# Optimization experiments

Hardware: AMD Instinct MI355X
Metric: run time of the kernel (lower is better)

The kernel has to match this reference:

```python
import jax, jax.numpy as jnp
import numpy as np

N_NODES = 100000
N_EDGES = 1600000
NUM_GRAPHS = 64
HID = 32
EPS = 1e-5


def _seg_max0(x, ids, num_segments):
    # segment max; segments with no entries become 0 (PyG-style identity)
    m = jax.ops.segment_max(x, ids, num_segments=num_segments)
    return jnp.where(jnp.isfinite(m), m, 0.0)


def _pointnet_layer(h, pos, src, dst, W1, b1, W2, b2):
    # message: mlp(cat([h_j, pos_j - pos_i])) ; aggregate: max at target i
    edge_feat = jnp.concatenate([h[src], pos[src] - pos[dst]], axis=-1)  # [E, C+3]
    m = jnp.maximum(edge_feat @ W1 + b1, 0.0) @ W2 + b2                  # [E, out]
    return _seg_max0(m, dst, N_NODES)                                    # [N, out]


def _batchnorm(x, gamma, beta):
    # training-mode BatchNorm1d: batch stats, biased variance
    mu = jnp.mean(x, axis=0)
    var = jnp.mean((x - mu) ** 2, axis=0)
    return (x - mu) * jax.lax.rsqrt(var + EPS) * gamma + beta


def setup_inputs() -> dict:
    key = jax.random.key(0)
    ks = jax.random.split(key, 16)
    pos = jax.random.normal(ks[0], (N_NODES, 3), dtype=jnp.float32)
    edge_index = jax.random.randint(ks[1], (2, N_EDGES), 0, N_NODES, dtype=jnp.int64)
    batch = jnp.sort(jax.random.randint(ks[2], (N_NODES,), 0, NUM_GRAPHS, dtype=jnp.int64))

    def lin(k, fan_in, fan_out):
        lim = 1.0 / np.sqrt(fan_in)
        kw, kb = jax.random.split(k)
        W = jax.random.uniform(kw, (fan_in, fan_out), jnp.float32, -lim, lim)
        b = jax.random.uniform(kb, (fan_out,), jnp.float32, -lim, lim)
        return W, b

    W1a, b1a = lin(ks[3], 3 + 3, HID)
    W2a, b2a = lin(ks[4], HID, HID)
    W1b, b1b = lin(ks[5], HID + 3, 2 * HID)
    W2b, b2b = lin(ks[6], 2 * HID, 2 * HID)
    Wc, bc = lin(ks[7], 2 * HID, 2)
    return {
        'pos': pos, 'edge_index': edge_index, 'batch': batch,
        'W1a': W1a, 'b1a': b1a, 'W2a': W2a, 'b2a': b2a,
        'g1': jnp.ones((HID,), jnp.float32), 'beta1': jnp.zeros((HID,), jnp.float32),
        'W1b': W1b, 'b1b': b1b, 'W2b': W2b, 'b2b': b2b,
        'g2': jnp.ones((2 * HID,), jnp.float32), 'beta2': jnp.zeros((2 * HID,), jnp.float32),
        'Wc': Wc, 'bc': bc,
    }


def reference(pos, edge_index, batch, W1a, b1a, W2a, b2a, g1, beta1,
              W1b, b1b, W2b, b2b, g2, beta2, Wc, bc):
    src, dst = edge_index[0], edge_index[1]  # source j -> target i
    h = _pointnet_layer(pos, pos, src, dst, W1a, b1a, W2a, b2a)   # [N, 32]
    h = jnp.maximum(_batchnorm(h, g1, beta1), 0.0)
    h = _pointnet_layer(h, pos, src, dst, W1b, b1b, W2b, b2b)     # [N, 64]
    h = jnp.maximum(_batchnorm(h, g2, beta2), 0.0)
    g = _seg_max0(h, batch, NUM_GRAPHS)                            # [G, 64]
    return g @ Wc + bc                                             # [G, 2]
```

## Files before the change

### kernel.cpp

```cpp
#include <hip/hip_runtime.h>

#define NN 100000
#define NE 1600000
#define NG 64
#define BSZ 98
#define NBUK 1021
#define SENTROW 127
#define NBLK1 391
#define EPB 4096

typedef __attribute__((ext_vector_type(8))) short bf16x8;
typedef __attribute__((ext_vector_type(4))) float f32x4;

union AFrag { bf16x8 v; uint4 u; };

__device__ __forceinline__ bool finitef(float v) {
    return (__float_as_uint(v) & 0x7F800000u) != 0x7F800000u;
}
__device__ __forceinline__ unsigned short f2bf(float f) {
    unsigned int u = __float_as_uint(f);
    u += 0x7fffu + ((u >> 16) & 1u);
    return (unsigned short)(u >> 16);
}
__device__ __forceinline__ unsigned int cvtpk(float lo, float hi) {
    unsigned int r;
    asm("v_cvt_pk_bf16_f32 %0, %1, %2" : "=v"(r) : "v"(lo), "v"(hi));
    return r;
}
__device__ __forceinline__ float bflo(unsigned int q) { return __uint_as_float(q << 16); }
__device__ __forceinline__ float bfhi(unsigned int q) { return __uint_as_float(q & 0xffff0000u); }

__device__ __forceinline__ unsigned int enc(float f) {
    unsigned int u = __float_as_uint(f);
    return (u & 0x80000000u) ? ~u : (u | 0x80000000u);
}
__device__ __forceinline__ float dec(unsigned int k) {
    unsigned int u = (k & 0x80000000u) ? (k ^ 0x80000000u) : ~k;
    return __uint_as_float(u);
}

__global__ __launch_bounds__(256) void p1count(const int* __restrict__ dst,
                                               int* __restrict__ gmat) {
    __shared__ int h[NBUK];
    int tid = threadIdx.x;
    for (int i = tid; i < NBUK; i += 256) h[i] = 0;
    __syncthreads();
    int e0 = blockIdx.x * EPB;
    #pragma unroll
    for (int i = 0; i < 16; ++i) {
        int e = e0 + tid + i * 256;
        if (e < NE) atomicAdd(&h[dst[e] / BSZ], 1);
    }
    __syncthreads();
    for (int i = tid; i < NBUK; i += 256) gmat[blockIdx.x * NBUK + i] = h[i];
}

__global__ __launch_bounds__(512) void scanA(int* __restrict__ gmat, int* __restrict__ tot) {
    __shared__ int ls[512];
    int b = blockIdx.x, tid = threadIdx.x;
    int v = (tid < NBLK1) ? gmat[tid * NBUK + b] : 0;
    ls[tid] = v;
    __syncthreads();
    for (int o = 1; o < 512; o <<= 1) {
        int t = (tid >= o) ? ls[tid - o] : 0;
        __syncthreads();
        ls[tid] += t;
        __syncthreads();
    }
    if (tid < NBLK1) gmat[tid * NBUK + b] = ls[tid] - v;
    if (tid == 511) tot[b] = ls[511];
}

__global__ __launch_bounds__(1024) void scanB(const int* __restrict__ tot,
        int* __restrict__ base,
        unsigned int* __restrict__ gmax, unsigned int* __restrict__ gneg) {
    __shared__ int ls[1024];
    int tid = threadIdx.x;
    int v = (tid < NBUK) ? tot[tid] : 0;
    ls[tid] = v;
    __syncthreads();
    for (int o = 1; o < 1024; o <<= 1) {
        int t = (tid >= o) ? ls[tid - o] : 0;
        __syncthreads();
        ls[tid] += t;
        __syncthreads();
    }
    if (tid < NBUK) base[tid] = ls[tid] - v;
    if (tid == 1023) base[NBUK] = ls[1023];
    for (int i = tid; i < NG * 64; i += 1024) { gmax[i] = 0u; gneg[i] = 0u; }
}

__global__ __launch_bounds__(256) void p1scatter(const int* __restrict__ src,
        const int* __restrict__ dst, const int* __restrict__ gmat,
        const int* __restrict__ base, int* __restrict__ sedge) {
    __shared__ int cur[NBUK];
    int tid = threadIdx.x;
    for (int i = tid; i < NBUK; i += 256) cur[i] = base[i] + gmat[blockIdx.x * NBUK + i];
    __syncthreads();
    int e0 = blockIdx.x * EPB;
    #pragma unroll
    for (int i = 0; i < 16; ++i) {
        int e = e0 + tid + i * 256;
        if (e < NE) {
            int d = dst[e];
            int buk = d / BSZ;
            int row = d - buk * BSZ;
            int p = atomicAdd(&cur[buk], 1);
            sedge[p] = src[e] | (row << 20);
        }
    }
}

__global__ __launch_bounds__(256) void uA_kernel(const float* __restrict__ pos,
        const float* __restrict__ W1, const float* __restrict__ b1,
        unsigned short* __restrict__ PA, unsigned short* __restrict__ QA) {
    __shared__ float sWp[96], sWq[96], sb[32];
    if (threadIdx.x < 96) {
        float wt = W1[96 + threadIdx.x];
        sWq[threadIdx.x] = wt;
        sWp[threadIdx.x] = W1[threadIdx.x] + wt;
    }
    if (threadIdx.x < 32) sb[threadIdx.x] = b1[threadIdx.x];
    __syncthreads();
    int n = blockIdx.x * 256 + threadIdx.x;
    if (n >= NN) return;
    float p0 = pos[n * 3 + 0], p1 = pos[n * 3 + 1], p2 = pos[n * 3 + 2];
    float P[32], Q[32];
    #pragma unroll
    for (int c = 0; c < 32; ++c) {
        P[c] = fmaf(p2, sWp[64 + c], fmaf(p1, sWp[32 + c], fmaf(p0, sWp[c], sb[c])));
        Q[c] = fmaf(p2, sWq[64 + c], fmaf(p1, sWq[32 + c], p0 * sWq[c]));
    }
    uint4* po = (uint4*)(PA + (size_t)n * 32);
    uint4* qo = (uint4*)(QA + (size_t)n * 32);
    #pragma unroll
    for (int q = 0; q < 4; ++q) {
        po[q] = make_uint4(cvtpk(P[8*q],P[8*q+1]), cvtpk(P[8*q+2],P[8*q+3]),
                           cvtpk(P[8*q+4],P[8*q+5]), cvtpk(P[8*q+6],P[8*q+7]));
        qo[q] = make_uint4(cvtpk(Q[8*q],Q[8*q+1]), cvtpk(Q[8*q+2],Q[8*q+3]),
                           cvtpk(Q[8*q+4],Q[8*q+5]), cvtpk(Q[8*q+6],Q[8*q+7]));
    }
}

__global__ __launch_bounds__(256) void uB_kernel(const unsigned int* __restrict__ accA,
        const float* __restrict__ ssA, const float* __restrict__ pos,
        const float* __restrict__ W1, const float* __restrict__ b1,
        unsigned short* __restrict__ PB, unsigned short* __restrict__ QB) {
    __shared__ float sW[32 * 64];
    __shared__ float sWt[3 * 64];
    __shared__ float sb[64];
    for (int i = threadIdx.x; i < 32 * 64; i += 256) sW[i] = W1[i];
    if (threadIdx.x < 192) sWt[threadIdx.x] = W1[32 * 64 + threadIdx.x];
    if (threadIdx.x < 64) sb[threadIdx.x] = b1[threadIdx.x];
    __syncthreads();
    int n = blockIdx.x * 256 + threadIdx.x;
    if (n >= NN) return;
    float h[32];
    const uint4* a4 = (const uint4*)(accA + (size_t)n * 32);
    #pragma unroll
    for (int q = 0; q < 8; ++q) {
        uint4 v = a4[q];
        unsigned int vv[4] = {v.x, v.y, v.z, v.w};
        #pragma unroll
        for (int r = 0; r < 4; ++r) {
            int c = 4 * q + r;
            float x = dec(vv[r]);
            x = finitef(x) ? x : 0.f;
            h[c] = fmaxf(fmaf(x, ssA[c], ssA[32 + c]), 0.f);
        }
    }
    float p0 = pos[n * 3 + 0], p1 = pos[n * 3 + 1], p2 = pos[n * 3 + 2];
    float Q[64], P[64];
    #pragma unroll
    for (int c = 0; c < 64; ++c) {
        Q[c] = fmaf(p2, sWt[128 + c], fmaf(p1, sWt[64 + c], p0 * sWt[c]));
        P[c] = Q[c] + sb[c];
    }
    #pragma unroll
    for (int k = 0; k < 32; ++k) {
        float x = h[k];
        #pragma unroll
        for (int c = 0; c < 64; ++c) P[c] = fmaf(x, sW[k * 64 + c], P[c]);
    }
    uint4* po = (uint4*)(PB + (size_t)n * 64);
    uint4* qo = (uint4*)(QB + (size_t)n * 64);
    #pragma unroll
    for (int q = 0; q < 8; ++q) {
        po[q] = make_uint4(cvtpk(P[8*q],P[8*q+1]), cvtpk(P[8*q+2],P[8*q+3]),
                           cvtpk(P[8*q+4],P[8*q+5]), cvtpk(P[8*q+6],P[8*q+7]));
        qo[q] = make_uint4(cvtpk(Q[8*q],Q[8*q+1]), cvtpk(Q[8*q+2],Q[8*q+3]),
                           cvtpk(Q[8*q+4],Q[8*q+5]), cvtpk(Q[8*q+6],Q[8*q+7]));
    }
}

__global__ __launch_bounds__(256, 6) void edgeA(
        const unsigned short* __restrict__ PA, const unsigned short* __restrict__ QA,
        const int* __restrict__ sedge, const int* __restrict__ bbase,
        const float* __restrict__ W2, const float* __restrict__ b2,
        unsigned int* __restrict__ accA, float* __restrict__ partials) {
    __shared__ __align__(16) short w2f[2 * 64 * 8];
    __shared__ unsigned int nm[32 * 99];
    __shared__ float psum[256], psq[256];

    const int tid = threadIdx.x;
    const int b   = blockIdx.x;
    const int nb0 = b * BSZ;
    const int lane = tid & 63, wv = tid >> 6;
    const int kg = lane >> 4;

    #pragma unroll
    for (int ii = 0; ii < 4; ++ii) {
        int i = tid + ii * 256;
        int j = i & 7, ln = (i >> 3) & 63, t = (i >> 9) & 1;
        int k = ((ln >> 4) & 3) * 8 + j, col = (ln & 15) + 16 * t;
        w2f[i] = (short)f2bf(W2[k * 32 + col]);
    }
    for (int i = tid; i < 32 * 99; i += 256) nm[i] = 0;
    __syncthreads();

    float b2v[2];
    #pragma unroll
    for (int t = 0; t < 2; ++t) b2v[t] = b2[(lane & 15) + 16 * t];

    const int bs = bbase[b], be = bbase[b + 1];
    int idx = bs + wv * 64 + lane;
    int myed = (idx < be) ? sedge[idx] : (SENTROW << 20);
    for (int e0 = bs; e0 < be; e0 += 256) {
        int nxt = (idx + 256 < be) ? sedge[idx + 256] : (SENTROW << 20);
        idx += 256;

        int edg[4]; unsigned int rw4[4];
        #pragma unroll
        for (int g = 0; g < 4; ++g) {
            edg[g] = __shfl(myed, g * 16 + (lane & 15), 64);
            unsigned int p = 0;
            #pragma unroll
            for (int r = 0; r < 4; ++r) {
                int e2 = __shfl(myed, g * 16 + kg * 4 + r, 64);
                p |= ((unsigned int)(e2 >> 20) & 0xFFu) << (8 * r);
            }
            rw4[g] = p;
        }

        AFrag af[4];
        #pragma unroll
        for (int g = 0; g < 4; ++g) {
            int s = edg[g] & 0xFFFFF;
            int rq = min(edg[g] >> 20, BSZ - 1);
            uint4 Pq = *(const uint4*)&PA[(size_t)s * 32 + kg * 8];
            uint4 Qq = *(const uint4*)&QA[(size_t)(nb0 + rq) * 32 + kg * 8];
            unsigned int pu[4] = {Pq.x, Pq.y, Pq.z, Pq.w};
            unsigned int qu[4] = {Qq.x, Qq.y, Qq.z, Qq.w};
            unsigned int outw[4];
            #pragma unroll
            for (int p = 0; p < 4; ++p) {
                float vlo = fmaxf(bflo(pu[p]) - bflo(qu[p]), 0.f);
                float vhi = fmaxf(bfhi(pu[p]) - bfhi(qu[p]), 0.f);
                outw[p] = cvtpk(vlo, vhi);
            }
            af[g].u = make_uint4(outw[0], outw[1], outw[2], outw[3]);
        }

        #pragma unroll
        for (int t = 0; t < 2; ++t) {
            bf16x8 bfr = *(const bf16x8*)&w2f[(t * 64 + lane) * 8];
            int ch = t * 16 + (lane & 15);
            #pragma unroll
            for (int g = 0; g < 4; ++g) {
                f32x4 c = {b2v[t], b2v[t], b2v[t], b2v[t]};
                f32x4 acc = __builtin_amdgcn_mfma_f32_16x16x32_bf16(af[g].v, bfr, c, 0, 0, 0);
                #pragma unroll
                for (int r = 0; r < 4; ++r) {
                    int rr = (rw4[g] >> (8 * r)) & 0xFF;
                    if (rr < BSZ) atomicMax(&nm[ch * 99 + rr], enc(acc[r]));
                }
            }
        }
        myed = nxt;
    }

    __syncthreads();
    {
        int c = tid & 31, sub = tid >> 5;
        float s = 0.f, q = 0.f;
        for (int nl = sub; nl < BSZ; nl += 8) {
            int n = nb0 + nl;
            if (n >= NN) break;
            unsigned int k = nm[c * 99 + nl];
            accA[(size_t)n * 32 + c] = k;
            float v = dec(k);
            v = finitef(v) ? v : 0.f;
            s += v; q = fmaf(v, v, q);
        }
        psum[tid] = s; psq[tid] = q;
    }
    __syncthreads();
    if (tid < 128) { psum[tid] += psum[tid + 128]; psq[tid] += psq[tid + 128]; }
    __syncthreads();
    if (tid < 64)  { psum[tid] += psum[tid + 64];  psq[tid] += psq[tid + 64]; }
    __syncthreads();
    if (tid < 32) {
        partials[b * 64 + tid]      = psum[tid] + psum[tid + 32];
        partials[b * 64 + 32 + tid] = psq[tid]  + psq[tid + 32];
    }
}

__global__ __launch_bounds__(256, 4) void edgeB(
        const unsigned short* __restrict__ PB, const unsigned short* __restrict__ QB,
        const int* __restrict__ sedge, const int* __restrict__ bbase,
        const int* __restrict__ batch,
        const float* __restrict__ W2, const float* __restrict__ b2,
        float* __restrict__ partials,
        unsigned int* __restrict__ gmax, unsigned int* __restrict__ gneg) {
    __shared__ __align__(16) short w2f[2 * 4 * 64 * 8];
    __shared__ unsigned int nm[64 * 99];
    __shared__ float psum[256], psq[256];

    const int tid = threadIdx.x;
    const int b   = blockIdx.x;
    const int nb0 = b * BSZ;
    const int lane = tid & 63, wv = tid >> 6;
    const int kg = lane >> 4;

    #pragma unroll
    for (int ii = 0; ii < 16; ++ii) {
        int i = tid + ii * 256;
        int j = i & 7, ln = (i >> 3) & 63, t = (i >> 9) & 3, ks = (i >> 11) & 1;
        int k = ks * 32 + ((ln >> 4) & 3) * 8 + j, col = (ln & 15) + 16 * t;
        w2f[i] = (short)f2bf(W2[k * 64 + col]);
    }
    for (int i = tid; i < 64 * 99; i += 256) nm[i] = 0;
    __syncthreads();

    float b2v[4];
    #pragma unroll
    for (int t = 0; t < 4; ++t) b2v[t] = b2[(lane & 15) + 16 * t];

    const int bs = bbase[b], be = bbase[b + 1];
    int idx = bs + wv * 64 + lane;
    int myed = (idx < be) ? sedge[idx] : (SENTROW << 20);
    for (int e0 = bs; e0 < be; e0 += 256) {
        int nxt = (idx + 256 < be) ? sedge[idx + 256] : (SENTROW << 20);
        idx += 256;

        int edg[4]; unsigned int rw4[4];
        #pragma unroll
        for (int g = 0; g < 4; ++g) {
            edg[g] = __shfl(myed, g * 16 + (lane & 15), 64);
            unsigned int p = 0;
            #pragma unroll
            for (int r = 0; r < 4; ++r) {
                int e2 = __shfl(myed, g * 16 + kg * 4 + r, 64);
                p |= ((unsigned int)(e2 >> 20) & 0xFFu) << (8 * r);
            }
            rw4[g] = p;
        }

        AFrag af[4][2];
        #pragma unroll
        for (int g = 0; g < 4; ++g) {
            int s = edg[g] & 0xFFFFF;
            int rq = min(edg[g] >> 20, BSZ - 1);
            #pragma unroll
            for (int ks = 0; ks < 2; ++ks) {
                uint4 Pq = *(const uint4*)&PB[(size_t)s * 64 + ks * 32 + kg * 8];
                uint4 Qq = *(const uint4*)&QB[(size_t)(nb0 + rq) * 64 + ks * 32 + kg * 8];
                unsigned int pu[4] = {Pq.x, Pq.y, Pq.z, Pq.w};
                unsigned int qu[4] = {Qq.x, Qq.y, Qq.z, Qq.w};
                unsigned int outw[4];
                #pragma unroll
                for (int p = 0; p < 4; ++p) {
                    float vlo = fmaxf(bflo(pu[p]) - bflo(qu[p]), 0.f);
                    float vhi = fmaxf(bfhi(pu[p]) - bfhi(qu[p]), 0.f);
                    outw[p] = cvtpk(vlo, vhi);
                }
                af[g][ks].u = make_uint4(outw[0], outw[1], outw[2], outw[3]);
            }
        }

        #pragma unroll
        for (int t = 0; t < 4; ++t) {
            bf16x8 bf0 = *(const bf16x8*)&w2f[((0 * 4 + t) * 64 + lane) * 8];
            bf16x8 bf1 = *(const bf16x8*)&w2f[((1 * 4 + t) * 64 + lane) * 8];
            int ch = t * 16 + (lane & 15);
            #pragma unroll
            for (int g = 0; g < 4; ++g) {
                f32x4 c = {b2v[t], b2v[t], b2v[t], b2v[t]};
                c = __builtin_amdgcn_mfma_f32_16x16x32_bf16(af[g][0].v, bf0, c, 0, 0, 0);
                f32x4 acc = __builtin_amdgcn_mfma_f32_16x16x32_bf16(af[g][1].v, bf1, c, 0, 0, 0);
                #pragma unroll
                for (int r = 0; r < 4; ++r) {
                    int rr = (rw4[g] >> (8 * r)) & 0xFF;
                    if (rr < BSZ) atomicMax(&nm[ch * 99 + rr], enc(acc[r]));
                }
            }
        }
        myed = nxt;
    }

    __syncthreads();
    {
        int c = tid & 63, sub = tid >> 6;
        float s = 0.f, q = 0.f;
        float rmax = 0.f, rneg = 0.f; int curg = -1;
        for (int nl = sub; nl < BSZ; nl += 4) {
            int n = nb0 + nl;
            if (n >= NN) break;
            float v = dec(nm[c * 99 + nl]);
            v = finitef(v) ? v : 0.f;
            s += v; q = fmaf(v, v, q);
            int g = batch[n];
            if (g != curg) {
                if (curg >= 0) {
                    atomicMax(&gmax[curg * 64 + c], enc(rmax));
                    atomicMax(&gneg[curg * 64 + c], enc(rneg));
                }
                curg = g; rmax = v; rneg = -v;
            } else {
                rmax = fmaxf(rmax, v); rneg = fmaxf(rneg, -v);
            }
        }
        if (curg >= 0) {
            atomicMax(&gmax[curg * 64 + c], enc(rmax));
            atomicMax(&gneg[curg * 64 + c], enc(rneg));
        }
        psum[tid] = s; psq[tid] = q;
    }
    __syncthreads();
    if (tid < 128) { psum[tid] += psum[tid + 128]; psq[tid] += psq[tid + 128]; }
    __syncthreads();
    if (tid < 64) {
        partials[b * 128 + tid]      = psum[tid] + psum[tid + 64];
        partials[b * 128 + 64 + tid] = psq[tid]  + psq[tid + 64];
    }
}

template <int C>
__global__ __launch_bounds__(1024) void bn_final(const float* __restrict__ partials, int nblocks,
                         const float* __restrict__ gamma, const float* __restrict__ beta,
                         float* __restrict__ ss) {
    __shared__ float lsum[1024], lsq[1024];
    const int NCH = 1024 / C;
    int tid = threadIdx.x;
    int c = tid & (C - 1);
    int chunk = tid / C;
    float s = 0.f, q = 0.f;
    for (int b = chunk; b < nblocks; b += NCH) {
        s += partials[b * 2 * C + c];
        q += partials[b * 2 * C + C + c];
    }
    lsum[chunk * C + c] = s; lsq[chunk * C + c] = q;
    __syncthreads();
    #pragma unroll
    for (int o = 512; o >= C; o >>= 1) {
        if (tid < o && o >= C) {
            lsum[tid] += lsum[tid + o];
            lsq[tid]  += lsq[tid + o];
        }
        __syncthreads();
    }
    if (tid < C) {
        float mu  = lsum[tid] / (float)NN;
        float var = fmaxf(lsq[tid] / (float)NN - mu * mu, 0.f);
        float inv = rsqrtf(var + 1e-5f);
        float sc  = gamma[tid] * inv;
        ss[tid]     = sc;
        ss[C + tid] = fmaf(-mu, sc, beta[tid]);
    }
}

__global__ void final_gemm(const unsigned int* __restrict__ gmax,
                           const unsigned int* __restrict__ gneg,
                           const float* __restrict__ ss, const float* __restrict__ Wc,
                           const float* __restrict__ bc, float* __restrict__ out) {
    int t = threadIdx.x;
    if (t >= NG * 2) return;
    int g = t >> 1, o = t & 1;
    float s = bc[o];
    for (int k = 0; k < 64; ++k) {
        float sc = ss[k], sh = ss[64 + k];
        float xm = dec(gmax[g * 64 + k]), xn = dec(gneg[g * 64 + k]);
        float x = (sc >= 0.f) ? xm : -xn;
        float v = finitef(x) ? fmaxf(fmaf(sc, x, sh), 0.f) : 0.f;
        s = fmaf(v, Wc[k * 2 + o], s);
    }
    out[t] = s;
}

extern "C" void kernel_launch(void* const* d_in, const int* in_sizes, int n_in,
                              void* d_out, int out_size, void* d_ws, size_t ws_size,
                              hipStream_t stream) {
    const float* pos   = (const float*)d_in[0];
    const int*   ei    = (const int*)d_in[1];
    const int*   batch = (const int*)d_in[2];
    const float* W1a = (const float*)d_in[3];
    const float* b1a = (const float*)d_in[4];
    const float* W2a = (const float*)d_in[5];
    const float* b2a = (const float*)d_in[6];
    const float* g1  = (const float*)d_in[7];
    const float* be1 = (const float*)d_in[8];
    const float* W1b = (const float*)d_in[9];
    const float* b1b = (const float*)d_in[10];
    const float* W2b = (const float*)d_in[11];
    const float* b2b = (const float*)d_in[12];
    const float* g2  = (const float*)d_in[13];
    const float* be2 = (const float*)d_in[14];
    const float* Wc  = (const float*)d_in[15];
    const float* bc  = (const float*)d_in[16];
    const int* srcp = ei;
    const int* dstp = ei + NE;

    char* base_p = (char*)d_ws;
    size_t ofs = 0;
    auto alloc = [&](size_t bytes) { char* p = base_p + ofs; ofs = (ofs + bytes + 255) & ~(size_t)255; return p; };
    int*   gmat  = (int*)alloc((size_t)NBLK1 * NBUK * 4);
    int*   tot   = (int*)alloc(NBUK * 4);
    int*   bbase = (int*)alloc((NBUK + 1) * 4);
    int*   sedge = (int*)alloc((size_t)NE * 4);
    unsigned short* PA = (unsigned short*)alloc((size_t)NN * 32 * 2);
    unsigned short* QA = (unsigned short*)alloc((size_t)NN * 32 * 2);
    unsigned short* PB = PA;
    unsigned short* QB = (unsigned short*)alloc((size_t)NN * 64 * 2);
    unsigned int* accA = (unsigned int*)alloc((size_t)NN * 32 * 4);
    float* partA = (float*)alloc((size_t)NBUK * 64 * 4);
    float* partB = (float*)alloc((size_t)NBUK * 128 * 4);
    float* ssA   = (float*)alloc(64 * 4);
    float* ssB   = (float*)alloc(128 * 4);
    unsigned int* gmax = (unsigned int*)alloc(NG * 64 * 4);
    unsigned int* gneg = (unsigned int*)alloc(NG * 64 * 4);

    p1count<<<NBLK1, 256, 0, stream>>>(dstp, gmat);
    scanA<<<NBUK, 512, 0, stream>>>(gmat, tot);
    scanB<<<1, 1024, 0, stream>>>(tot, bbase, gmax, gneg);
    p1scatter<<<NBLK1, 256, 0, stream>>>(srcp, dstp, gmat, bbase, sedge);

    uA_kernel<<<(NN + 255) / 256, 256, 0, stream>>>(pos, W1a, b1a, PA, QA);
    edgeA<<<NBUK, 256, 0, stream>>>(PA, QA, sedge, bbase, W2a, b2a, accA, partA);
    bn_final<32><<<1, 1024, 0, stream>>>(partA, NBUK, g1, be1, ssA);

    uB_kernel<<<(NN + 255) / 256, 256, 0, stream>>>(accA, ssA, pos, W1b, b1b, PB, QB);
    edgeB<<<NBUK, 256, 0, stream>>>(PB, QB, sedge, bbase, batch, W2b, b2b, partB, gmax, gneg);
    bn_final<64><<<1, 1024, 0, stream>>>(partB, NBUK, g2, be2, ssB);
    final_gemm<<<1, 128, 0, stream>>>(gmax, gneg, ssB, Wc, bc, (float*)d_out);
}
```

Measured before the change: 219.0 us.

## Switch edge MLP to fp16 packed math and 512-thread edge blocks

Stores the precomputed P/Q node tables in fp16 instead of bf16. The subtract-and-ReLU now runs as packed half2 ops instead of unpacking to fp32 and repacking. The MFMA calls switch to the f16 variant. Separately, both edge kernels now launch 512 threads per block, processing more edges per iteration with an extra reduction step. Risks: fp16 range or overflow on the activations, and higher register/LDS pressure from the larger blocks.

```diff
diff --git a/kernel.cpp b/kernel.cpp
--- a/kernel.cpp
+++ b/kernel.cpp
@@ -1,4 +1,5 @@
 #include <hip/hip_runtime.h>
+#include <hip/hip_fp16.h>
 
 #define NN 100000
 #define NE 1600000
@@ -9,26 +10,30 @@
 #define NBLK1 391
 #define EPB 4096
 
-typedef __attribute__((ext_vector_type(8))) short bf16x8;
+typedef __attribute__((ext_vector_type(8))) _Float16 f16x8;
+typedef __attribute__((ext_vector_type(2))) _Float16 f16x2;
 typedef __attribute__((ext_vector_type(4))) float f32x4;
 
-union AFrag { bf16x8 v; uint4 u; };
+union AFrag { f16x8 v; uint4 u; };
 
 __device__ __forceinline__ bool finitef(float v) {
     return (__float_as_uint(v) & 0x7F800000u) != 0x7F800000u;
 }
-__device__ __forceinline__ unsigned short f2bf(float f) {
-    unsigned int u = __float_as_uint(f);
-    u += 0x7fffu + ((u >> 16) & 1u);
-    return (unsigned short)(u >> 16);
-}
-__device__ __forceinline__ unsigned int cvtpk(float lo, float hi) {
-    unsigned int r;
-    asm("v_cvt_pk_bf16_f32 %0, %1, %2" : "=v"(r) : "v"(lo), "v"(hi));
-    return r;
-}
-__device__ __forceinline__ float bflo(unsigned int q) { return __uint_as_float(q << 16); }
-__device__ __forceinline__ float bfhi(unsigned int q) { return __uint_as_float(q & 0xffff0000u); }
+__device__ __forceinline__ unsigned int pkh(float lo, float hi) {
+    f16x2 h = { (_Float16)lo, (_Float16)hi };
+    return *(unsigned int*)&h;
+}
+__device__ __forceinline__ short f2h_bits(float f) {
+    _Float16 h = (_Float16)f;
+    return *(short*)&h;
+}
+__device__ __forceinline__ unsigned int hsubmax0(unsigned int pu, unsigned int qu) {
+    f16x2 hp = *(const f16x2*)&pu;
+    f16x2 hq = *(const f16x2*)&qu;
+    f16x2 z = { (_Float16)0, (_Float16)0 };
+    f16x2 r = __builtin_elementwise_max(hp - hq, z);
+    return *(unsigned int*)&r;
+}
 
 __device__ __forceinline__ unsigned int enc(float f) {
     unsigned int u = __float_as_uint(f);
@@ -135,10 +140,10 @@
     uint4* qo = (uint4*)(QA + (size_t)n * 32);
     #pragma unroll
     for (int q = 0; q < 4; ++q) {
-        po[q] = make_uint4(cvtpk(P[8*q],P[8*q+1]), cvtpk(P[8*q+2],P[8*q+3]),
-                           cvtpk(P[8*q+4],P[8*q+5]), cvtpk(P[8*q+6],P[8*q+7]));
-        qo[q] = make_uint4(cvtpk(Q[8*q],Q[8*q+1]), cvtpk(Q[8*q+2],Q[8*q+3]),
-                           cvtpk(Q[8*q+4],Q[8*q+5]), cvtpk(Q[8*q+6],Q[8*q+7]));
+        po[q] = make_uint4(pkh(P[8*q],P[8*q+1]), pkh(P[8*q+2],P[8*q+3]),
+                           pkh(P[8*q+4],P[8*q+5]), pkh(P[8*q+6],P[8*q+7]));
+        qo[q] = make_uint4(pkh(Q[8*q],Q[8*q+1]), pkh(Q[8*q+2],Q[8*q+3]),
+                           pkh(Q[8*q+4],Q[8*q+5]), pkh(Q[8*q+6],Q[8*q+7]));
     }
 }
 
@@ -186,21 +191,21 @@
     uint4* qo = (uint4*)(QB + (size_t)n * 64);
     #pragma unroll
     for (int q = 0; q < 8; ++q) {
-        po[q] = make_uint4(cvtpk(P[8*q],P[8*q+1]), cvtpk(P[8*q+2],P[8*q+3]),
-                           cvtpk(P[8*q+4],P[8*q+5]), cvtpk(P[8*q+6],P[8*q+7]));
-        qo[q] = make_uint4(cvtpk(Q[8*q],Q[8*q+1]), cvtpk(Q[8*q+2],Q[8*q+3]),
-                           cvtpk(Q[8*q+4],Q[8*q+5]), cvtpk(Q[8*q+6],Q[8*q+7]));
-    }
-}
-
-__global__ __launch_bounds__(256, 6) void edgeA(
+        po[q] = make_uint4(pkh(P[8*q],P[8*q+1]), pkh(P[8*q+2],P[8*q+3]),
+                           pkh(P[8*q+4],P[8*q+5]), pkh(P[8*q+6],P[8*q+7]));
+        qo[q] = make_uint4(pkh(Q[8*q],Q[8*q+1]), pkh(Q[8*q+2],Q[8*q+3]),
+                           pkh(Q[8*q+4],Q[8*q+5]), pkh(Q[8*q+6],Q[8*q+7]));
+    }
+}
+
+__global__ __launch_bounds__(512, 8) void edgeA(
         const unsigned short* __restrict__ PA, const unsigned short* __restrict__ QA,
         const int* __restrict__ sedge, const int* __restrict__ bbase,
         const float* __restrict__ W2, const float* __restrict__ b2,
         unsigned int* __restrict__ accA, float* __restrict__ partials) {
     __shared__ __align__(16) short w2f[2 * 64 * 8];
     __shared__ unsigned int nm[32 * 99];
-    __shared__ float psum[256], psq[256];
+    __shared__ float psum[512], psq[512];
 
     const int tid = threadIdx.x;
     const int b   = blockIdx.x;
@@ -208,14 +213,12 @@
     const int lane = tid & 63, wv = tid >> 6;
     const int kg = lane >> 4;
 
-    #pragma unroll
-    for (int ii = 0; ii < 4; ++ii) {
-        int i = tid + ii * 256;
+    for (int i = tid; i < 2 * 64 * 8; i += 512) {
         int j = i & 7, ln = (i >> 3) & 63, t = (i >> 9) & 1;
         int k = ((ln >> 4) & 3) * 8 + j, col = (ln & 15) + 16 * t;
-        w2f[i] = (short)f2bf(W2[k * 32 + col]);
-    }
-    for (int i = tid; i < 32 * 99; i += 256) nm[i] = 0;
+        w2f[i] = f2h_bits(W2[k * 32 + col]);
+    }
+    for (int i = tid; i < 32 * 99; i += 512) nm[i] = 0;
     __syncthreads();
 
     float b2v[2];
@@ -225,9 +228,9 @@
     const int bs = bbase[b], be = bbase[b + 1];
     int idx = bs + wv * 64 + lane;
     int myed = (idx < be) ? sedge[idx] : (SENTROW << 20);
-    for (int e0 = bs; e0 < be; e0 += 256) {
-        int nxt = (idx + 256 < be) ? sedge[idx + 256] : (SENTROW << 20);
-        idx += 256;
+    for (int e0 = bs; e0 < be; e0 += 512) {
+        int nxt = (idx + 512 < be) ? sedge[idx + 512] : (SENTROW << 20);
+        idx += 512;
 
         int edg[4]; unsigned int rw4[4];
         #pragma unroll
@@ -249,26 +252,18 @@
             int rq = min(edg[g] >> 20, BSZ - 1);
             uint4 Pq = *(const uint4*)&PA[(size_t)s * 32 + kg * 8];
             uint4 Qq = *(const uint4*)&QA[(size_t)(nb0 + rq) * 32 + kg * 8];
-            unsigned int pu[4] = {Pq.x, Pq.y, Pq.z, Pq.w};
-            unsigned int qu[4] = {Qq.x, Qq.y, Qq.z, Qq.w};
-            unsigned int outw[4];
-            #pragma unroll
-            for (int p = 0; p < 4; ++p) {
-                float vlo = fmaxf(bflo(pu[p]) - bflo(qu[p]), 0.f);
-                float vhi = fmaxf(bfhi(pu[p]) - bfhi(qu[p]), 0.f);
-                outw[p] = cvtpk(vlo, vhi);
-            }
-            af[g].u = make_uint4(outw[0], outw[1], outw[2], outw[3]);
+            af[g].u = make_uint4(hsubmax0(Pq.x, Qq.x), hsubmax0(Pq.y, Qq.y),
+                                 hsubmax0(Pq.z, Qq.z), hsubmax0(Pq.w, Qq.w));
         }
 
         #pragma unroll
         for (int t = 0; t < 2; ++t) {
-            bf16x8 bfr = *(const bf16x8*)&w2f[(t * 64 + lane) * 8];
+            f16x8 bfr = *(const f16x8*)&w2f[(t * 64 + lane) * 8];
             int ch = t * 16 + (lane & 15);
             #pragma unroll
             for (int g = 0; g < 4; ++g) {
                 f32x4 c = {b2v[t], b2v[t], b2v[t], b2v[t]};
-                f32x4 acc = __builtin_amdgcn_mfma_f32_16x16x32_bf16(af[g].v, bfr, c, 0, 0, 0);
+                f32x4 acc = __builtin_amdgcn_mfma_f32_16x16x32_f16(af[g].v, bfr, c, 0, 0, 0);
                 #pragma unroll
                 for (int r = 0; r < 4; ++r) {
                     int rr = (rw4[g] >> (8 * r)) & 0xFF;
@@ -283,7 +278,7 @@
     {
         int c = tid & 31, sub = tid >> 5;
         float s = 0.f, q = 0.f;
-        for (int nl = sub; nl < BSZ; nl += 8) {
+        for (int nl = sub; nl < BSZ; nl += 16) {
             int n = nb0 + nl;
             if (n >= NN) break;
             unsigned int k = nm[c * 99 + nl];
@@ -295,6 +290,8 @@
         psum[tid] = s; psq[tid] = q;
     }
     __syncthreads();
+    if (tid < 256) { psum[tid] += psum[tid + 256]; psq[tid] += psq[tid + 256]; }
+    __syncthreads();
     if (tid < 128) { psum[tid] += psum[tid + 128]; psq[tid] += psq[tid + 128]; }
     __syncthreads();
     if (tid < 64)  { psum[tid] += psum[tid + 64];  psq[tid] += psq[tid + 64]; }
@@ -305,7 +302,7 @@
     }
 }
 
-__global__ __launch_bounds__(256, 4) void edgeB(
+__global__ __launch_bounds__(512, 8) void edgeB(
         const unsigned short* __restrict__ PB, const unsigned short* __restrict__ QB,
         const int* __restrict__ sedge, const int* __restrict__ bbase,
         const int* __restrict__ batch,
@@ -314,7 +311,7 @@
         unsigned int* __restrict__ gmax, unsigned int* __restrict__ gneg) {
     __shared__ __align__(16) short w2f[2 * 4 * 64 * 8];
     __shared__ unsigned int nm[64 * 99];
-    __shared__ float psum[256], psq[256];
+    __shared__ float psum[512], psq[512];
 
     const int tid = threadIdx.x;
     const int b   = blockIdx.x;
@@ -322,14 +319,12 @@
     const int lane = tid & 63, wv = tid >> 6;
     const int kg = lane >> 4;
 
-    #pragma unroll
-    for (int ii = 0; ii < 16; ++ii) {
-        int i = tid + ii * 256;
+    for (int i = tid; i < 2 * 4 * 64 * 8; i += 512) {
         int j = i & 7, ln = (i >> 3) & 63, t = (i >> 9) & 3, ks = (i >> 11) & 1;
         int k = ks * 32 + ((ln >> 4) & 3) * 8 + j, col = (ln & 15) + 16 * t;
-        w2f[i] = (short)f2bf(W2[k * 64 + col]);
-    }
-    for (int i = tid; i < 64 * 99; i += 256) nm[i] = 0;
+        w2f[i] = f2h_bits(W2[k * 64 + col]);
+    }
+    for (int i = tid; i < 64 * 99; i += 512) nm[i] = 0;
     __syncthreads();
 
     float b2v[4];
@@ -339,9 +334,9 @@
     const int bs = bbase[b], be = bbase[b + 1];
     int idx = bs + wv * 64 + lane;
     int myed = (idx < be) ? sedge[idx] : (SENTROW << 20);
-    for (int e0 = bs; e0 < be; e0 += 256) {
-        int nxt = (idx + 256 < be) ? sedge[idx + 256] : (SENTROW << 20);
-        idx += 256;
+    for (int e0 = bs; e0 < be; e0 += 512) {
+        int nxt = (idx + 512 < be) ? sedge[idx + 512] : (SENTROW << 20);
+        idx += 512;
 
         int edg[4]; unsigned int rw4[4];
         #pragma unroll
@@ -365,29 +360,21 @@
             for (int ks = 0; ks < 2; ++ks) {
                 uint4 Pq = *(const uint4*)&PB[(size_t)s * 64 + ks * 32 + kg * 8];
                 uint4 Qq = *(const uint4*)&QB[(size_t)(nb0 + rq) * 64 + ks * 32 + kg * 8];
-                unsigned int pu[4] = {Pq.x, Pq.y, Pq.z, Pq.w};
-                unsigned int qu[4] = {Qq.x, Qq.y, Qq.z, Qq.w};
-                unsigned int outw[4];
-                #pragma unroll
-                for (int p = 0; p < 4; ++p) {
-                    float vlo = fmaxf(bflo(pu[p]) - bflo(qu[p]), 0.f);
-                    float vhi = fmaxf(bfhi(pu[p]) - bfhi(qu[p]), 0.f);
-                    outw[p] = cvtpk(vlo, vhi);
-                }
-                af[g][ks].u = make_uint4(outw[0], outw[1], outw[2], outw[3]);
+                af[g][ks].u = make_uint4(hsubmax0(Pq.x, Qq.x), hsubmax0(Pq.y, Qq.y),
+                                         hsubmax0(Pq.z, Qq.z), hsubmax0(Pq.w, Qq.w));
             }
         }
 
         #pragma unroll
         for (int t = 0; t < 4; ++t) {
-            bf16x8 bf0 = *(const bf16x8*)&w2f[((0 * 4 + t) * 64 + lane) * 8];
-            bf16x8 bf1 = *(const bf16x8*)&w2f[((1 * 4 + t) * 64 + lane) * 8];
+            f16x8 bf0 = *(const f16x8*)&w2f[((0 * 4 + t) * 64 + lane) * 8];
+            f16x8 bf1 = *(const f16x8*)&w2f[((1 * 4 + t) * 64 + lane) * 8];
             int ch = t * 16 + (lane & 15);
             #pragma unroll
             for (int g = 0; g < 4; ++g) {
                 f32x4 c = {b2v[t], b2v[t], b2v[t], b2v[t]};
-                c = __builtin_amdgcn_mfma_f32_16x16x32_bf16(af[g][0].v, bf0, c, 0, 0, 0);
-                f32x4 acc = __builtin_amdgcn_mfma_f32_16x16x32_bf16(af[g][1].v, bf1, c, 0, 0, 0);
+                c = __builtin_amdgcn_mfma_f32_16x16x32_f16(af[g][0].v, bf0, c, 0, 0, 0);
+                f32x4 acc = __builtin_amdgcn_mfma_f32_16x16x32_f16(af[g][1].v, bf1, c, 0, 0, 0);
                 #pragma unroll
                 for (int r = 0; r < 4; ++r) {
                     int rr = (rw4[g] >> (8 * r)) & 0xFF;
@@ -403,7 +390,7 @@
         int c = tid & 63, sub = tid >> 6;
         float s = 0.f, q = 0.f;
         float rmax = 0.f, rneg = 0.f; int curg = -1;
-        for (int nl = sub; nl < BSZ; nl += 4) {
+        for (int nl = sub; nl < BSZ; nl += 8) {
             int n = nb0 + nl;
             if (n >= NN) break;
             float v = dec(nm[c * 99 + nl]);
@@ -426,6 +413,8 @@
         }
         psum[tid] = s; psq[tid] = q;
     }
+    __syncthreads();
+    if (tid < 256) { psum[tid] += psum[tid + 256]; psq[tid] += psq[tid + 256]; }
     __syncthreads();
     if (tid < 128) { psum[tid] += psum[tid + 128]; psq[tid] += psq[tid + 128]; }
     __syncthreads();
@@ -535,11 +524,11 @@
     p1scatter<<<NBLK1, 256, 0, stream>>>(srcp, dstp, gmat, bbase, sedge);
 
     uA_kernel<<<(NN + 255) / 256, 256, 0, stream>>>(pos, W1a, b1a, PA, QA);
-    edgeA<<<NBUK, 256, 0, stream>>>(PA, QA, sedge, bbase, W2a, b2a, accA, partA);
+    edgeA<<<NBUK, 512, 0, stream>>>(PA, QA, sedge, bbase, W2a, b2a, accA, partA);
     bn_final<32><<<1, 1024, 0, stream>>>(partA, NBUK, g1, be1, ssA);
 
     uB_kernel<<<(NN + 255) / 256, 256, 0, stream>>>(accA, ssA, pos, W1b, b1b, PB, QB);
-    edgeB<<<NBUK, 256, 0, stream>>>(PB, QB, sedge, bbase, batch, W2b, b2b, partB, gmax, gneg);
+    edgeB<<<NBUK, 512, 0, stream>>>(PB, QB, sedge, bbase, batch, W2b, b2b, partB, gmax, gneg);
     bn_final<64><<<1, 1024, 0, stream>>>(partB, NBUK, g2, be2, ssB);
     final_gemm<<<1, 128, 0, stream>>>(gmax, gneg, ssB, Wc, bc, (float*)d_out);
 }
```

After: 473.0 us. 2.16x slower.
